# Optimization experiments

Hardware: AMD Instinct MI355X
Metric: run time of the kernel (lower is better)

The kernel has to match this reference:

```python
import jax, jax.numpy as jnp
import numpy as np

EPS = 1e-6
NUM_HEADS = 12


def _layernorm(x, eps=EPS):
    m = jnp.mean(x, axis=-1, keepdims=True)
    v = jnp.var(x, axis=-1, keepdims=True)
    return (x - m) * jax.lax.rsqrt(v + eps)


def _rmsnorm(x, w, eps=EPS):
    ms = jnp.mean(jnp.square(x), axis=-1, keepdims=True)
    return x * jax.lax.rsqrt(ms + eps) * w


def _rope_interleaved(x, cos, sin):
    # x: [B, L, H, hd]; cos/sin: [L, hd//2]; is_neox_style=False (interleaved pairs)
    x1 = x[..., 0::2]
    x2 = x[..., 1::2]
    c = cos[None, :, None, :]
    s = sin[None, :, None, :]
    o1 = x1 * c - x2 * s
    o2 = x1 * s + x2 * c
    return jnp.stack([o1, o2], axis=-1).reshape(x.shape)


def _attention(q, k, v, mask=None):
    # q: [B, Lq, H, hd], k/v: [B, Lk, H, hd]
    hd = q.shape[-1]
    scale = 1.0 / jnp.sqrt(jnp.asarray(hd, q.dtype))
    scores = jnp.einsum('blhd,bmhd->bhlm', q, k) * scale
    if mask is not None:
        scores = jnp.where(mask[None, None], scores, jnp.finfo(scores.dtype).min)
    p = jax.nn.softmax(scores, axis=-1)
    return jnp.einsum('bhlm,bmhd->blhd', p, v)


def setup_inputs() -> dict:
    key = jax.random.key(0)
    B, F, FS, D, FF, LC = 1, 2, 1560, 1536, 8960, 512
    L = F * FS
    hd = D // NUM_HEADS
    ks = jax.random.split(key, 32)
    i = iter(range(32))
    n = lambda shape, s=0.02: jax.random.normal(ks[next(i)], shape, jnp.float32) * s
    inp = {
        'hidden_states': n((B, L, D), 1.0),
        'encoder_hidden_states': n((B, LC, D), 1.0),
        'temb': n((B, F, 6, D), 1.0),
    }
    pos = jnp.arange(L, dtype=jnp.float32)
    inv = 1.0 / (10000.0 ** (jnp.arange(hd // 2, dtype=jnp.float32) / (hd // 2)))
    ang = pos[:, None] * inv[None, :]
    inp['cos'] = jnp.cos(ang)
    inp['sin'] = jnp.sin(ang)
    fidx = jnp.arange(L) // FS
    inp['attn_mask'] = fidx[:, None] >= fidx[None, :]  # frame-level block-causal
    # params
    inp['sst'] = n((1, 6, D), 1.0 / np.sqrt(D))
    for name in ['wq', 'wk', 'wv', 'wo']:
        inp[name] = n((D, D))
    for name in ['bq', 'bk', 'bv', 'bo']:
        inp[name] = jnp.zeros((D,), jnp.float32)
    inp['nq_w'] = jnp.ones((D,), jnp.float32)
    inp['nk_w'] = jnp.ones((D,), jnp.float32)
    inp['ln2_g'] = jnp.ones((D,), jnp.float32)
    inp['ln2_b'] = jnp.zeros((D,), jnp.float32)
    for name in ['cwq', 'cwk', 'cwv', 'cwo']:
        inp[name] = n((D, D))
    for name in ['cbq', 'cbk', 'cbv', 'cbo']:
        inp[name] = jnp.zeros((D,), jnp.float32)
    inp['cnq_w'] = jnp.ones((D,), jnp.float32)
    inp['cnk_w'] = jnp.ones((D,), jnp.float32)
    inp['w1'] = n((D, FF))
    inp['b1'] = jnp.zeros((FF,), jnp.float32)
    inp['w2'] = n((FF, D))
    inp['b2'] = jnp.zeros((D,), jnp.float32)
    return inp


def reference(hidden_states, encoder_hidden_states, temb, cos, sin, attn_mask,
              sst, wq, bq, wk, bk, wv, bv, wo, bo, nq_w, nk_w, ln2_g, ln2_b,
              cwq, cbq, cwk, cbk, cwv, cbv, cwo, cbo, cnq_w, cnk_w,
              w1, b1, w2, b2):
    B, L, D = hidden_states.shape
    F = temb.shape[1]
    FS = L // F
    H = NUM_HEADS
    hd = D // H

    e = sst[:, None] + temb  # [B, F, 6, D]
    shift_msa, scale_msa, gate_msa = e[:, :, 0], e[:, :, 1], e[:, :, 2]
    c_shift, c_scale, c_gate = e[:, :, 3], e[:, :, 4], e[:, :, 5]

    # --- self attention ---
    nh = _layernorm(hidden_states).reshape(B, F, FS, D)
    nh = (nh * (1.0 + scale_msa[:, :, None]) + shift_msa[:, :, None]).reshape(B, L, D)
    q = _rmsnorm(nh @ wq + bq, nq_w).reshape(B, L, H, hd)
    k = _rmsnorm(nh @ wk + bk, nk_w).reshape(B, L, H, hd)
    v = (nh @ wv + bv).reshape(B, L, H, hd)
    q = _rope_interleaved(q, cos, sin)
    k = _rope_interleaved(k, cos, sin)
    attn_out = _attention(q, k, v, attn_mask).reshape(B, L, D) @ wo + bo

    h = hidden_states + (attn_out.reshape(B, F, FS, D) * gate_msa[:, :, None]).reshape(B, L, D)
    norm_h = _layernorm(h) * ln2_g + ln2_b  # null shift/scale

    # --- cross attention ---
    LC = encoder_hidden_states.shape[1]
    cq = _rmsnorm(norm_h @ cwq + cbq, cnq_w).reshape(B, L, H, hd)
    ck = _rmsnorm(encoder_hidden_states @ cwk + cbk, cnk_w).reshape(B, LC, H, hd)
    cv = (encoder_hidden_states @ cwv + cbv).reshape(B, LC, H, hd)
    cross_out = _attention(cq, ck, cv).reshape(B, L, D) @ cwo + cbo

    h = h + cross_out  # gate = 1
    norm_h = _layernorm(h).reshape(B, F, FS, D)
    norm_h = (norm_h * (1.0 + c_scale[:, :, None]) + c_shift[:, :, None]).reshape(B, L, D)

    # --- ffn ---
    ff = jax.nn.gelu(norm_h @ w1 + b1, approximate=True) @ w2 + b2
    h = h + (ff.reshape(B, F, FS, D) * c_gate[:, :, None]).reshape(B, L, D)
    return h
```

## Files before the change

### kernel.cpp

```cpp
#include <hip/hip_runtime.h>
#include <hip/hip_bf16.h>
#include <math.h>

typedef __bf16 bf16;
typedef __bf16 bf16x8 __attribute__((ext_vector_type(8)));
typedef float  f32x4  __attribute__((ext_vector_type(4)));
typedef unsigned int u32;

#define DMODEL 1536
#define NHEADS 12
#define HD 128
#define HDH 64

__device__ __forceinline__ void async16(const void* g, void* l) {
  __builtin_amdgcn_global_load_lds((const __attribute__((address_space(1))) u32*)g,
                                   (__attribute__((address_space(3))) u32*)l, 16, 0, 0);
}

__device__ inline void block_reduce2(float& a, float& b) {
  __shared__ float sa[4], sb[4];
  #pragma unroll
  for (int off = 32; off; off >>= 1) {
    a += __shfl_xor(a, off);
    b += __shfl_xor(b, off);
  }
  int w = threadIdx.x >> 6;
  if ((threadIdx.x & 63) == 0) { sa[w] = a; sb[w] = b; }
  __syncthreads();
  a = sa[0] + sa[1] + sa[2] + sa[3];
  b = sb[0] + sb[1] + sb[2] + sb[3];
  __syncthreads();
}

__global__ __launch_bounds__(256)
void ln_kernel(const float* __restrict__ X, bf16* __restrict__ Y,
               const float* __restrict__ sst, const float* __restrict__ temb,
               const float* __restrict__ g, const float* __restrict__ bvec,
               int jshift, int jscale, int FS, int mode)
{
  int row = blockIdx.x;
  const float* x = X + (size_t)row * DMODEL;
  float v[6];
  float s1 = 0.f, s2 = 0.f;
  #pragma unroll
  for (int i = 0; i < 6; i++) {
    float t = x[threadIdx.x + i * 256];
    v[i] = t; s1 += t; s2 += t * t;
  }
  block_reduce2(s1, s2);
  float mean = s1 * (1.f / DMODEL);
  float var  = s2 * (1.f / DMODEL) - mean * mean;
  float rs = rsqrtf(var + 1e-6f);
  int f = row / FS;
  bf16* y = Y + (size_t)row * DMODEL;
  #pragma unroll
  for (int i = 0; i < 6; i++) {
    int d = threadIdx.x + i * 256;
    float t = (v[i] - mean) * rs;
    float o;
    if (mode == 0) {
      float sc = sst[jscale * DMODEL + d] + temb[(f * 6 + jscale) * DMODEL + d];
      float sh = sst[jshift * DMODEL + d] + temb[(f * 6 + jshift) * DMODEL + d];
      o = t * (1.f + sc) + sh;
    } else {
      o = t * g[d] + bvec[d];
    }
    y[d] = (bf16)o;
  }
}

__global__ __launch_bounds__(256)
void rms_rope_kernel(const float* __restrict__ P, int S, long long MN,
                     const bf16* __restrict__ Xb, int RS, int CO,
                     const float* __restrict__ bias, bf16* __restrict__ Y,
                     const float* __restrict__ w,
                     const float* __restrict__ cosb, const float* __restrict__ sinb,
                     int dorope, float oscale)
{
  __shared__ float rowbuf[DMODEL];
  int row = blockIdx.x;
  float v[6];
  float s2 = 0.f, dummy = 0.f;
  if (Xb) {
    const bf16* x = Xb + (size_t)row * RS + CO;
    #pragma unroll
    for (int i = 0; i < 6; i++) {
      int d = threadIdx.x + i * 256;
      float t = (float)x[d];
      v[i] = t; rowbuf[d] = t; s2 += t * t;
    }
  } else {
    const float* x = P + (size_t)row * RS + CO;
    #pragma unroll
    for (int i = 0; i < 6; i++) {
      int d = threadIdx.x + i * 256;
      float t = bias[d];
      for (int s = 0; s < S; s++) t += x[(size_t)s * MN + d];
      v[i] = t; rowbuf[d] = t; s2 += t * t;
    }
  }
  __syncthreads();
  block_reduce2(s2, dummy);
  float rs = rsqrtf(s2 * (1.f / DMODEL) + 1e-6f) * oscale;
  bf16* y = Y + (size_t)row * DMODEL;
  if (dorope) {
    #pragma unroll
    for (int i = 0; i < 3; i++) {
      int p = threadIdx.x + i * 256;
      int d0 = 2 * p, d1 = 2 * p + 1;
      float y0 = rowbuf[d0] * rs * w[d0];
      float y1 = rowbuf[d1] * rs * w[d1];
      int ih = p & 63;
      float c = cosb[(size_t)row * HDH + ih];
      float s = sinb[(size_t)row * HDH + ih];
      y[d0] = (bf16)(y0 * c - y1 * s);
      y[d1] = (bf16)(y0 * s + y1 * c);
    }
  } else {
    #pragma unroll
    for (int i = 0; i < 6; i++) {
      int d = threadIdx.x + i * 256;
      y[d] = (bf16)(v[i] * rs * w[d]);
    }
  }
}

__global__ __launch_bounds__(256)
void wt_kernel(const float* __restrict__ W, bf16* __restrict__ Wt, int K, int N)
{
  __shared__ float T[32][33];
  int k0 = blockIdx.x * 32, n0 = blockIdx.y * 32;
  int tx = threadIdx.x & 31, ty = threadIdx.x >> 5;
  #pragma unroll
  for (int i = 0; i < 4; i++)
    T[ty + 8 * i][tx] = W[(size_t)(k0 + ty + 8 * i) * N + n0 + tx];
  __syncthreads();
  #pragma unroll
  for (int i = 0; i < 4; i++)
    Wt[(size_t)(n0 + ty + 8 * i) * K + k0 + tx] = (bf16)T[tx][ty + 8 * i];
}

__global__ __launch_bounds__(256)
void catbias_kernel(float* __restrict__ bqkv, const float* __restrict__ bq,
                    const float* __restrict__ bk, const float* __restrict__ bv,
                    float* __restrict__ cbkv, const float* __restrict__ cbk,
                    const float* __restrict__ cbv)
{
  int i = blockIdx.x * 256 + threadIdx.x;
  if (i < DMODEL) {
    bqkv[i] = bq[i]; bqkv[DMODEL + i] = bk[i]; bqkv[2 * DMODEL + i] = bv[i];
    cbkv[i] = cbk[i]; cbkv[DMODEL + i] = cbv[i];
  }
}

__global__ __launch_bounds__(256)
void gemm_bt(const bf16* __restrict__ A, const bf16* __restrict__ Bt,
             const float* __restrict__ bias, float* __restrict__ Cf,
             bf16* __restrict__ Cb, int M, int N, int K, int act,
             int Ks, long long MN)
{
  __shared__ bf16 As[128 * 32];
  __shared__ bf16 Bs[128 * 32];
  int tid = threadIdx.x, lane = tid & 63, w = tid >> 6;
  int wm = w >> 1, wn = w & 1;
  int l16 = lane & 15, quad = lane >> 4;

  int gx = (M + 127) >> 7, gy = N >> 7;
  int per_panel = gx << 3;
  int bid = blockIdx.x;
  int panel = bid / per_panel;
  int rem = bid - panel * per_panel;
  int pc0 = panel << 3;
  int ncols = gy - pc0; if (ncols > 8) ncols = 8;
  int by = pc0 + rem % ncols;
  int bx = rem / ncols;
  int bm = bx * 128, bn = by * 128;

  int kb0 = blockIdx.y * Ks;

  int rl = lane >> 2;
  int kk = (lane & 3) * 8;
  int r0 = (2 * w) * 16 + rl, r1 = (2 * w + 1) * 16 + rl;
  int am0 = bm + r0; if (am0 > M - 1) am0 = M - 1;
  int am1 = bm + r1; if (am1 > M - 1) am1 = M - 1;
  const bf16* a0 = A + (size_t)am0 * K + kk;
  const bf16* a1 = A + (size_t)am1 * K + kk;
  const bf16* b0 = Bt + (size_t)(bn + r0) * K + kk;
  const bf16* b1 = Bt + (size_t)(bn + r1) * K + kk;
  bf16* lA0 = As + (2 * w) * 512; bf16* lA1 = As + (2 * w + 1) * 512;
  bf16* lB0 = Bs + (2 * w) * 512; bf16* lB1 = Bs + (2 * w + 1) * 512;

  f32x4 acc[4][4] = {};
  int kend = kb0 + Ks;
  for (int k0 = kb0; k0 < kend; k0 += 32) {
    async16(a0 + k0, lA0);
    async16(a1 + k0, lA1);
    async16(b0 + k0, lB0);
    async16(b1 + k0, lB1);
    __syncthreads();
    bf16x8 af[4], bfv[4];
    #pragma unroll
    for (int mi = 0; mi < 4; mi++)
      af[mi] = *(const bf16x8*)&As[(wm * 64 + mi * 16 + l16) * 32 + quad * 8];
    #pragma unroll
    for (int ni = 0; ni < 4; ni++)
      bfv[ni] = *(const bf16x8*)&Bs[(wn * 64 + ni * 16 + l16) * 32 + quad * 8];
    #pragma unroll
    for (int mi = 0; mi < 4; mi++)
      #pragma unroll
      for (int ni = 0; ni < 4; ni++)
        acc[mi][ni] = __builtin_amdgcn_mfma_f32_16x16x32_bf16(af[mi], bfv[ni], acc[mi][ni], 0, 0, 0);
    __syncthreads();
  }
  float* Cfo = Cf ? Cf + (size_t)blockIdx.y * MN : nullptr;
  #pragma unroll
  for (int mi = 0; mi < 4; mi++) {
    #pragma unroll
    for (int r = 0; r < 4; r++) {
      int m = bm + wm * 64 + mi * 16 + quad * 4 + r;
      if (m < M) {
        #pragma unroll
        for (int ni = 0; ni < 4; ni++) {
          int n = bn + wn * 64 + ni * 16 + l16;
          float val = acc[mi][ni][r] + (bias ? bias[n] : 0.f);
          if (act == 1) {
            float u = val + 0.044715f * val * val * val;
            float z = 1.5957691216057308f * u;
            val = val / (1.f + __expf(-z));
          }
          if (Cfo) Cfo[(size_t)m * N + n] = val;
          else     Cb[(size_t)m * N + n] = (bf16)val;
        }
      }
    }
  }
}

__global__ __launch_bounds__(256)
void transposev_kernel(const bf16* __restrict__ Xb, int RS, int CO,
                       bf16* __restrict__ Vt, int L)
{
  __shared__ bf16 T[64][65];
  int l0 = blockIdx.x * 64, n0 = blockIdx.y * 64;
  int tid = threadIdx.x;
  int r = tid >> 2;
  int c8 = (tid & 3) * 16;
  int lc = l0 + r; if (lc > L - 1) lc = L - 1;
  const bf16* src = Xb + (size_t)lc * RS + CO + n0 + c8;
  #pragma unroll
  for (int i = 0; i < 16; i++) T[r][c8 + i] = src[i];
  __syncthreads();
  #pragma unroll
  for (int i = 0; i < 16; i++) {
    int l = l0 + c8 + i;
    if (l < L) Vt[(size_t)(n0 + r) * L + l] = T[c8 + i][r];
  }
}

__global__ __launch_bounds__(256)
void flash2_kernel(const bf16* __restrict__ Q, const bf16* __restrict__ Kg,
                   const bf16* __restrict__ Vt, bf16* __restrict__ O,
                   int Lq, int Lk, int FS, int causal, int nqb)
{
  __shared__ bf16 Kt[64 * 128];
  __shared__ bf16 Vtile[128 * 64];
  __shared__ bf16 Pl[4][16][72];
  int tid = threadIdx.x, lane = tid & 63, w = tid >> 6;
  int l16 = lane & 15, quad = lane >> 4;
  int bid = blockIdx.x;
  int h = bid % NHEADS;
  int qb = nqb - 1 - (bid / NHEADS);
  int q0b = qb * 64;
  int q0w = q0b + w * 16;

  int qrow = q0w + l16; if (qrow > Lq - 1) qrow = Lq - 1;
  const bf16* qbase = Q + (size_t)qrow * DMODEL + h * HD + quad * 8;
  bf16x8 qf[4];
  #pragma unroll
  for (int dc = 0; dc < 4; dc++) qf[dc] = *(const bf16x8*)(qbase + dc * 32);

  int kvrow[4];
  int kvmin_w = Lk, kv_end = Lk;
  if (causal) {
    #pragma unroll
    for (int r = 0; r < 4; r++) {
      int qr = q0w + quad * 4 + r; if (qr > Lq - 1) qr = Lq - 1;
      kvrow[r] = (qr / FS + 1) * FS;
    }
    int q0c = q0w; if (q0c > Lq - 1) q0c = Lq - 1;
    kvmin_w = (q0c / FS + 1) * FS;
    int qlast = q0b + 63; if (qlast > Lq - 1) qlast = Lq - 1;
    kv_end = (qlast / FS + 1) * FS;
    if (kv_end > Lk) kv_end = Lk;
  }

  f32x4 acc_o[8] = {};
  float m_i[4], l_i[4];
  #pragma unroll
  for (int r = 0; r < 4; r++) { m_i[r] = -1e30f; l_i[r] = 0.f; }

  for (int kb = 0; kb < kv_end; kb += 64) {
    #pragma unroll
    for (int j = 0; j < 4; j++) {
      int u = w * 256 + j * 64 + lane;
      int row = u >> 4;
      int c = (u & 15) ^ (row & 15);
      int krow = kb + row; if (krow > Lk - 1) krow = Lk - 1;
      async16(Kg + (size_t)krow * DMODEL + h * HD + c * 8,
              Kt + (size_t)(w * 256 + j * 64) * 8);
    }
    #pragma unroll
    for (int j = 0; j < 4; j++) {
      int u = w * 256 + j * 64 + lane;
      int row = u >> 3;
      int c = (u & 7) ^ (row & 7);
      async16(Vt + (size_t)(h * HD + row) * Lk + kb + c * 8,
              Vtile + (size_t)(w * 256 + j * 64) * 8);
    }
    __syncthreads();

    f32x4 s[4] = {};
    #pragma unroll
    for (int nk = 0; nk < 4; nk++) {
      #pragma unroll
      for (int dc = 0; dc < 4; dc++) {
        bf16x8 kf = *(const bf16x8*)&Kt[(((nk * 16 + l16) << 4) + ((4 * dc + quad) ^ l16)) * 8];
        s[nk] = __builtin_amdgcn_mfma_f32_16x16x32_bf16(qf[dc], kf, s[nk], 0, 0, 0);
      }
    }

    bool need_mask = causal && (kb + 64 > kvmin_w);
    float p[4][4];
    #pragma unroll
    for (int r = 0; r < 4; r++) {
      #pragma unroll
      for (int nk = 0; nk < 4; nk++) {
        float sv = s[nk][r];
        if (need_mask && (kb + nk * 16 + l16 >= kvrow[r])) sv = -1e30f;
        p[nk][r] = sv;
      }
      float bm = fmaxf(fmaxf(p[0][r], p[1][r]), fmaxf(p[2][r], p[3][r]));
      #pragma unroll
      for (int off = 8; off; off >>= 1) bm = fmaxf(bm, __shfl_xor(bm, off));
      float mn = fmaxf(m_i[r], bm);
      float alpha = __expf(m_i[r] - mn);
      m_i[r] = mn;
      float ps = 0.f;
      #pragma unroll
      for (int nk = 0; nk < 4; nk++) {
        float e = __expf(p[nk][r] - mn);
        p[nk][r] = e; ps += e;
      }
      #pragma unroll
      for (int off = 8; off; off >>= 1) ps += __shfl_xor(ps, off);
      l_i[r] = l_i[r] * alpha + ps;
      #pragma unroll
      for (int t = 0; t < 8; t++) acc_o[t][r] *= alpha;
    }

    #pragma unroll
    for (int nk = 0; nk < 4; nk++)
      #pragma unroll
      for (int r = 0; r < 4; r++)
        Pl[w][quad * 4 + r][nk * 16 + l16] = (bf16)p[nk][r];
    __threadfence_block();
    bf16x8 pf0 = *(const bf16x8*)&Pl[w][l16][quad * 8];
    bf16x8 pf1 = *(const bf16x8*)&Pl[w][l16][32 + quad * 8];

    #pragma unroll
    for (int t = 0; t < 8; t++) {
      bf16x8 vf0 = *(const bf16x8*)&Vtile[(((t * 16 + l16) << 3) + ((quad) ^ (l16 & 7))) * 8];
      bf16x8 vf1 = *(const bf16x8*)&Vtile[(((t * 16 + l16) << 3) + ((4 + quad) ^ (l16 & 7))) * 8];
      acc_o[t] = __builtin_amdgcn_mfma_f32_16x16x32_bf16(pf0, vf0, acc_o[t], 0, 0, 0);
      acc_o[t] = __builtin_amdgcn_mfma_f32_16x16x32_bf16(pf1, vf1, acc_o[t], 0, 0, 0);
    }
    __syncthreads();
  }

  #pragma unroll
  for (int r = 0; r < 4; r++) {
    int m = q0w + quad * 4 + r;
    if (m < Lq) {
      float inv = 1.f / l_i[r];
      bf16* obase = O + (size_t)m * DMODEL + h * HD;
      #pragma unroll
      for (int t = 0; t < 8; t++)
        obase[t * 16 + l16] = (bf16)(acc_o[t][r] * inv);
    }
  }
}

__global__ __launch_bounds__(256)
void modresid_kernel(const float* __restrict__ base, const float* __restrict__ P,
                     int S, long long MN, const float* __restrict__ bias,
                     float* __restrict__ out,
                     const float* __restrict__ sst, const float* __restrict__ temb,
                     int jg, int FS, long long total)
{
  long long i = (long long)blockIdx.x * 256 + threadIdx.x;
  if (i >= total) return;
  int d = (int)(i % DMODEL);
  int f = (int)((i / DMODEL) / FS);
  float g = sst[jg * DMODEL + d] + temb[(f * 6 + jg) * DMODEL + d];
  float v = bias[d];
  for (int s = 0; s < S; s++) v += P[(size_t)s * MN + i];
  out[i] = base[i] + v * g;
}

__global__ __launch_bounds__(256)
void addf_kernel(float* __restrict__ h, const float* __restrict__ P,
                 int S, long long MN, const float* __restrict__ bias, long long total)
{
  long long i = (long long)blockIdx.x * 256 + threadIdx.x;
  if (i >= total) return;
  int d = (int)(i % DMODEL);
  float v = bias[d];
  for (int s = 0; s < S; s++) v += P[(size_t)s * MN + i];
  h[i] += v;
}

__global__ __launch_bounds__(256)
void cast_kernel(const float* __restrict__ x, bf16* __restrict__ y, long long total)
{
  long long i = (long long)blockIdx.x * 256 + threadIdx.x;
  if (i < total) y[i] = (bf16)x[i];
}

extern "C" void kernel_launch(void* const* d_in, const int* in_sizes, int n_in,
                              void* d_out, int out_size, void* d_ws, size_t ws_size,
                              hipStream_t stream)
{
  const float* hs   = (const float*)d_in[0];
  const float* enc  = (const float*)d_in[1];
  const float* temb = (const float*)d_in[2];
  const float* cosb = (const float*)d_in[3];
  const float* sinb = (const float*)d_in[4];
  const float* sst  = (const float*)d_in[6];
  const float* wq = (const float*)d_in[7];
  const float* wk = (const float*)d_in[8];
  const float* wv = (const float*)d_in[9];
  const float* wo = (const float*)d_in[10];
  const float* bq = (const float*)d_in[11];
  const float* bk = (const float*)d_in[12];
  const float* bv = (const float*)d_in[13];
  const float* bo = (const float*)d_in[14];
  const float* nq_w = (const float*)d_in[15];
  const float* nk_w = (const float*)d_in[16];
  const float* ln2_g = (const float*)d_in[17];
  const float* ln2_b = (const float*)d_in[18];
  const float* cwq = (const float*)d_in[19];
  const float* cwk = (const float*)d_in[20];
  const float* cwv = (const float*)d_in[21];
  const float* cwo = (const float*)d_in[22];
  const float* cbq = (const float*)d_in[23];
  const float* cbk = (const float*)d_in[24];
  const float* cbv = (const float*)d_in[25];
  const float* cbo = (const float*)d_in[26];
  const float* cnq_w = (const float*)d_in[27];
  const float* cnk_w = (const float*)d_in[28];
  const float* w1 = (const float*)d_in[29];
  const float* b1 = (const float*)d_in[30];
  const float* w2 = (const float*)d_in[31];
  const float* b2 = (const float*)d_in[32];

  int L  = in_sizes[0] / DMODEL;
  int LC = in_sizes[1] / DMODEL;
  int F  = in_sizes[2] / (6 * DMODEL);
  int FS = L / F;
  int FF = in_sizes[30];
  long long LD = (long long)L * DMODEL;
  float* outp = (float*)d_out;
  int N3 = 3 * DMODEL, N2 = 2 * DMODEL;

  char* p = (char*)d_ws;
  auto alloc = [&](size_t bytes) -> char* {
    char* r = p; p += (bytes + 255) & ~(size_t)255; return r;
  };
  size_t DD = (size_t)DMODEL * DMODEL;
  bf16* wqkv_t = (bf16*)alloc(DD * 3 * 2);
  bf16* wto_t  = (bf16*)alloc(DD * 2);
  bf16* cwq_t  = (bf16*)alloc(DD * 2);
  bf16* cwkv_t = (bf16*)alloc(DD * 2 * 2);
  bf16* cwo_t  = (bf16*)alloc(DD * 2);
  bf16* w1t = (bf16*)alloc((size_t)DMODEL * FF * 2);
  bf16* w2t = (bf16*)alloc((size_t)DMODEL * FF * 2);
  float* bqkv = (float*)alloc((size_t)N3 * 4);
  float* cbkv = (float*)alloc((size_t)N2 * 4);
  float* hbuf = (float*)alloc((size_t)LD * 4);
  bf16* nh   = (bf16*)alloc((size_t)LD * 2);
  bf16* qb   = (bf16*)alloc((size_t)LD * 2);
  bf16* kb   = (bf16*)alloc((size_t)LD * 2);
  bf16* ab   = (bf16*)alloc((size_t)LD * 2);
  bf16* vtc  = (bf16*)alloc((size_t)LC * DMODEL * 2);
  bf16* encb = (bf16*)alloc((size_t)LC * DMODEL * 2);
  char* BIG1 = alloc((size_t)L * FF * 2);
  bf16* qkvb = (bf16*)BIG1;
  bf16* ckvb = (bf16*)BIG1;
  bf16* ffb  = (bf16*)BIG1;
  char* BIG2 = alloc((size_t)LD * 2 * 4);
  bf16* vtb = (bf16*)BIG2;
  float* Pp = (float*)BIG2;
  (void)ws_size; (void)n_in; (void)out_size;

  dim3 gWdd(DMODEL / 32, DMODEL / 32);
  wt_kernel<<<gWdd, 256, 0, stream>>>(wq, wqkv_t, DMODEL, DMODEL);
  wt_kernel<<<gWdd, 256, 0, stream>>>(wk, wqkv_t + DD, DMODEL, DMODEL);
  wt_kernel<<<gWdd, 256, 0, stream>>>(wv, wqkv_t + 2 * DD, DMODEL, DMODEL);
  wt_kernel<<<gWdd, 256, 0, stream>>>(wo, wto_t, DMODEL, DMODEL);
  wt_kernel<<<gWdd, 256, 0, stream>>>(cwq, cwq_t, DMODEL, DMODEL);
  wt_kernel<<<gWdd, 256, 0, stream>>>(cwk, cwkv_t, DMODEL, DMODEL);
  wt_kernel<<<gWdd, 256, 0, stream>>>(cwv, cwkv_t + DD, DMODEL, DMODEL);
  wt_kernel<<<gWdd, 256, 0, stream>>>(cwo, cwo_t, DMODEL, DMODEL);
  wt_kernel<<<dim3(DMODEL / 32, FF / 32), 256, 0, stream>>>(w1, w1t, DMODEL, FF);
  wt_kernel<<<dim3(FF / 32, DMODEL / 32), 256, 0, stream>>>(w2, w2t, FF, DMODEL);
  catbias_kernel<<<6, 256, 0, stream>>>(bqkv, bq, bk, bv, cbkv, cbk, cbv);

  int gxL = (L + 127) / 128, gxC = (LC + 127) / 128;
  int ewg = (int)((LD + 255) / 256);
  int nqb = (L + 63) / 64;
  const float qs = 0.08838834764831845f;

  ln_kernel<<<L, 256, 0, stream>>>(hs, nh, sst, temb, nullptr, nullptr, 0, 1, FS, 0);
  gemm_bt<<<dim3(gxL * (N3 / 128), 1), 256, 0, stream>>>(nh, wqkv_t, bqkv, nullptr, qkvb,
                                                         L, N3, DMODEL, 0, DMODEL, 0);
  rms_rope_kernel<<<L, 256, 0, stream>>>(nullptr, 0, 0, qkvb, N3, 0, nullptr, qb, nq_w, cosb, sinb, 1, qs);
  rms_rope_kernel<<<L, 256, 0, stream>>>(nullptr, 0, 0, qkvb, N3, DMODEL, nullptr, kb, nk_w, cosb, sinb, 1, 1.0f);
  transposev_kernel<<<dim3((L + 63) / 64, DMODEL / 64), 256, 0, stream>>>(qkvb, N3, 2 * DMODEL, vtb, L);
  flash2_kernel<<<NHEADS * nqb, 256, 0, stream>>>(qb, kb, vtb, ab, L, L, FS, 1, nqb);
  gemm_bt<<<dim3(gxL * (DMODEL / 128), 2), 256, 0, stream>>>(ab, wto_t, nullptr, Pp, nullptr,
                                                             L, DMODEL, DMODEL, 0, DMODEL / 2, LD);
  modresid_kernel<<<ewg, 256, 0, stream>>>(hs, Pp, 2, LD, bo, hbuf, sst, temb, 2, FS, LD);
  ln_kernel<<<L, 256, 0, stream>>>(hbuf, nh, nullptr, nullptr, ln2_g, ln2_b, 0, 0, FS, 1);
  gemm_bt<<<dim3(gxL * (DMODEL / 128), 2), 256, 0, stream>>>(nh, cwq_t, nullptr, Pp, nullptr,
                                                             L, DMODEL, DMODEL, 0, DMODEL / 2, LD);
  rms_rope_kernel<<<L, 256, 0, stream>>>(Pp, 2, LD, nullptr, DMODEL, 0, cbq, qb, cnq_w, nullptr, nullptr, 0, qs);
  cast_kernel<<<(int)(((long long)LC * DMODEL + 255) / 256), 256, 0, stream>>>(enc, encb, (long long)LC * DMODEL);
  gemm_bt<<<dim3(gxC * (N2 / 128), 1), 256, 0, stream>>>(encb, cwkv_t, cbkv, nullptr, ckvb,
                                                         LC, N2, DMODEL, 0, DMODEL, 0);
  rms_rope_kernel<<<LC, 256, 0, stream>>>(nullptr, 0, 0, ckvb, N2, 0, nullptr, kb, cnk_w, nullptr, nullptr, 0, 1.0f);
  transposev_kernel<<<dim3((LC + 63) / 64, DMODEL / 64), 256, 0, stream>>>(ckvb, N2, DMODEL, vtc, LC);
  flash2_kernel<<<NHEADS * nqb, 256, 0, stream>>>(qb, kb, vtc, ab, L, LC, FS, 0, nqb);
  gemm_bt<<<dim3(gxL * (DMODEL / 128), 2), 256, 0, stream>>>(ab, cwo_t, nullptr, Pp, nullptr,
                                                             L, DMODEL, DMODEL, 0, DMODEL / 2, LD);
  addf_kernel<<<ewg, 256, 0, stream>>>(hbuf, Pp, 2, LD, cbo, LD);
  ln_kernel<<<L, 256, 0, stream>>>(hbuf, nh, sst, temb, nullptr, nullptr, 3, 4, FS, 0);
  gemm_bt<<<dim3(gxL * (FF / 128), 1), 256, 0, stream>>>(nh, w1t, b1, nullptr, ffb,
                                                         L, FF, DMODEL, 1, DMODEL, 0);
  gemm_bt<<<dim3(gxL * (DMODEL / 128), 2), 256, 0, stream>>>(ffb, w2t, nullptr, Pp, nullptr,
                                                             L, DMODEL, FF, 0, FF / 2, LD);
  modresid_kernel<<<ewg, 256, 0, stream>>>(hbuf, Pp, 2, LD, b2, outp, sst, temb, 5, FS, LD);
}
```

Baseline: 1.226 ms.

## Add 256x256-tile pipelined MFMA GEMM and route all large GEMMs through it

Introduces a 512-thread GEMM kernel with 256x256 output tiles and 64-wide K steps. It double-buffers A/B tiles in LDS using async global-to-LDS loads with an XOR swizzle, and interleaves the loads with MFMA phases under s_setprio and explicit waitcnt/barriers. All QKV, projection and FFN GEMMs now use it instead of the 128x128 kernel. The larger tiles give more data reuse per block but produce far fewer blocks, some wasted rows since 3120 does not divide by 256, and about 128KB of LDS per block, so occupancy and CU fill may suffer on the D=1536 GEMMs.

```diff
diff --git a/kernel.cpp b/kernel.cpp
--- a/kernel.cpp
+++ b/kernel.cpp
@@ -218,6 +218,162 @@
     #pragma unroll
     for (int r = 0; r < 4; r++) {
       int m = bm + wm * 64 + mi * 16 + quad * 4 + r;
+      if (m < M) {
+        #pragma unroll
+        for (int ni = 0; ni < 4; ni++) {
+          int n = bn + wn * 64 + ni * 16 + l16;
+          float val = acc[mi][ni][r] + (bias ? bias[n] : 0.f);
+          if (act == 1) {
+            float u = val + 0.044715f * val * val * val;
+            float z = 1.5957691216057308f * u;
+            val = val / (1.f + __expf(-z));
+          }
+          if (Cfo) Cfo[(size_t)m * N + n] = val;
+          else     Cb[(size_t)m * N + n] = (bf16)val;
+        }
+      }
+    }
+  }
+}
+
+__global__ __launch_bounds__(512, 2)
+void gemm256(const bf16* __restrict__ A, const bf16* __restrict__ Bt,
+             const float* __restrict__ bias, float* __restrict__ Cf,
+             bf16* __restrict__ Cb, int M, int N, int K, int act,
+             int Ks, long long MN)
+{
+  __shared__ bf16 LDS[2][2][128 * 128];
+  int tid = threadIdx.x, lane = tid & 63, w = tid >> 6;
+  int wm = w >> 2, wn = w & 3;
+  int l16 = lane & 15, quad = lane >> 4;
+
+  int gmx = (M + 255) >> 8;
+  int bx = blockIdx.x % gmx, by = blockIdx.x / gmx;
+  int bm = bx << 8, bn = by << 8;
+  int kb0 = blockIdx.y * Ks;
+  int NT = Ks >> 6;
+
+  int aro = (l16 * 64 + quad * 16) ^ ((l16 >> 3) << 5);
+  const char* A0r = (const char*)&LDS[0][0][0] + wm * 16384 + aro;
+  const char* A1r = (const char*)&LDS[1][0][0] + wm * 16384 + aro;
+  const char* B0r = (const char*)&LDS[0][1][0] + wn * 8192 + aro;
+  const char* B1r = (const char*)&LDS[1][1][0] + wn * 8192 + aro;
+
+  int srl = lane >> 2;
+  int sc16 = (lane & 3) ^ (((lane >> 5) & 1) << 1);
+  int Mm1 = M - 1, Nm1 = N - 1;
+  int ga0 = bm + w * 16 + srl;        if (ga0 > Mm1) ga0 = Mm1;
+  int ga1 = bm + 128 + w * 16 + srl;  if (ga1 > Mm1) ga1 = Mm1;
+  int gb0 = bn + w * 16 + srl;        if (gb0 > Nm1) gb0 = Nm1;
+  int gb1 = bn + 128 + w * 16 + srl;  if (gb1 > Nm1) gb1 = Nm1;
+  const bf16* Ag0 = A + (size_t)ga0 * K + sc16 * 8;
+  const bf16* Ag1 = A + (size_t)ga1 * K + sc16 * 8;
+  const bf16* Bg0 = Bt + (size_t)gb0 * K + sc16 * 8;
+  const bf16* Bg1 = Bt + (size_t)gb1 * K + sc16 * 8;
+  char* wA0[2] = { (char*)&LDS[0][0][0] + w * 2048, (char*)&LDS[1][0][0] + w * 2048 };
+  char* wA1[2] = { wA0[0] + 16384, wA0[1] + 16384 };
+  char* wB0[2] = { (char*)&LDS[0][1][0] + w * 2048, (char*)&LDS[1][1][0] + w * 2048 };
+  char* wB1[2] = { wB0[0] + 16384, wB0[1] + 16384 };
+
+#define STG(src, kk_, dst) do { const bf16* _s = (src) + (kk_); \
+    async16(_s, (dst)); async16(_s + 32, (dst) + 1024); } while (0)
+#define MFMA_(d, a, b) d = __builtin_amdgcn_mfma_f32_16x16x32_bf16(a, b, d, 0, 0, 0)
+
+  STG(Ag0, kb0, wA0[0]); STG(Ag1, kb0, wA1[0]);
+  STG(Bg0, kb0, wB0[0]); STG(Bg1, kb0, wB1[0]);
+  if (NT > 1) {
+    STG(Bg0, kb0 + 64, wB0[1]); STG(Bg1, kb0 + 64, wB1[1]);
+    asm volatile("s_waitcnt vmcnt(4)" ::: "memory");
+  } else {
+    asm volatile("s_waitcnt vmcnt(0)" ::: "memory");
+  }
+  __builtin_amdgcn_s_barrier();
+
+  f32x4 acc[8][4] = {};
+  for (int t = 0; t < NT; ++t) {
+    int b = t & 1;
+    const char* Ab = b ? A1r : A0r;
+    const char* Bb = b ? B1r : B0r;
+    int kt1 = kb0 + (t + 1) * 64;
+    int kt2 = kt1 + 64;
+    bool st1 = (t + 1) < NT, st2 = (t + 2) < NT;
+
+    bf16x8 a0[8], b0v[4];
+    #pragma unroll
+    for (int i = 0; i < 8; i++) a0[i] = *(const bf16x8*)(Ab + i * 1024);
+    #pragma unroll
+    for (int i = 0; i < 4; i++) b0v[i] = *(const bf16x8*)(Bb + i * 1024);
+    if (st1) STG(Ag0, kt1, wA0[b ^ 1]);
+    __builtin_amdgcn_s_barrier();
+    asm volatile("s_waitcnt lgkmcnt(0)" ::: "memory");
+    __builtin_amdgcn_s_setprio(1);
+    #pragma unroll
+    for (int mi = 0; mi < 4; mi++)
+      #pragma unroll
+      for (int ni = 0; ni < 2; ni++) {
+        MFMA_(acc[mi][ni], a0[mi * 2],     b0v[ni * 2]);
+        MFMA_(acc[mi][ni], a0[mi * 2 + 1], b0v[ni * 2 + 1]);
+      }
+    __builtin_amdgcn_s_setprio(0);
+    __builtin_amdgcn_s_barrier();
+
+    bf16x8 b1v[4];
+    #pragma unroll
+    for (int i = 0; i < 4; i++) b1v[i] = *(const bf16x8*)(Bb + (4 + i) * 1024);
+    if (st1) STG(Ag1, kt1, wA1[b ^ 1]);
+    __builtin_amdgcn_s_barrier();
+    asm volatile("s_waitcnt lgkmcnt(0)" ::: "memory");
+    __builtin_amdgcn_s_setprio(1);
+    #pragma unroll
+    for (int mi = 0; mi < 4; mi++)
+      #pragma unroll
+      for (int ni = 0; ni < 2; ni++) {
+        MFMA_(acc[mi][2 + ni], a0[mi * 2],     b1v[ni * 2]);
+        MFMA_(acc[mi][2 + ni], a0[mi * 2 + 1], b1v[ni * 2 + 1]);
+      }
+    __builtin_amdgcn_s_setprio(0);
+    __builtin_amdgcn_s_barrier();
+
+    bf16x8 a1[8];
+    #pragma unroll
+    for (int i = 0; i < 8; i++) a1[i] = *(const bf16x8*)(Ab + (8 + i) * 1024);
+    if (st2) STG(Bg0, kt2, wB0[b]);
+    __builtin_amdgcn_s_barrier();
+    asm volatile("s_waitcnt lgkmcnt(0)" ::: "memory");
+    __builtin_amdgcn_s_setprio(1);
+    #pragma unroll
+    for (int mi = 0; mi < 4; mi++)
+      #pragma unroll
+      for (int ni = 0; ni < 2; ni++) {
+        MFMA_(acc[4 + mi][2 + ni], a1[mi * 2],     b1v[ni * 2]);
+        MFMA_(acc[4 + mi][2 + ni], a1[mi * 2 + 1], b1v[ni * 2 + 1]);
+      }
+    __builtin_amdgcn_s_setprio(0);
+    __builtin_amdgcn_s_barrier();
+
+    if (st2) STG(Bg1, kt2, wB1[b]);
+    __builtin_amdgcn_s_setprio(1);
+    #pragma unroll
+    for (int mi = 0; mi < 4; mi++)
+      #pragma unroll
+      for (int ni = 0; ni < 2; ni++) {
+        MFMA_(acc[4 + mi][ni], a1[mi * 2],     b0v[ni * 2]);
+        MFMA_(acc[4 + mi][ni], a1[mi * 2 + 1], b0v[ni * 2 + 1]);
+      }
+    __builtin_amdgcn_s_setprio(0);
+    if (st2)      { asm volatile("s_waitcnt vmcnt(4)" ::: "memory"); }
+    else if (st1) { asm volatile("s_waitcnt vmcnt(0)" ::: "memory"); }
+    __builtin_amdgcn_s_barrier();
+  }
+#undef STG
+#undef MFMA_
+
+  float* Cfo = Cf ? Cf + (size_t)blockIdx.y * MN : nullptr;
+  #pragma unroll
+  for (int mi = 0; mi < 8; mi++) {
+    #pragma unroll
+    for (int r = 0; r < 4; r++) {
+      int m = bm + wm * 128 + mi * 16 + quad * 4 + r;
       if (m < M) {
         #pragma unroll
         for (int ni = 0; ni < 4; ni++) {
@@ -515,23 +671,24 @@
   wt_kernel<<<dim3(FF / 32, DMODEL / 32), 256, 0, stream>>>(w2, w2t, FF, DMODEL);
   catbias_kernel<<<6, 256, 0, stream>>>(bqkv, bq, bk, bv, cbkv, cbk, cbv);
 
-  int gxL = (L + 127) / 128, gxC = (LC + 127) / 128;
+  int gxC = (LC + 127) / 128;
+  int gmx = (L + 255) / 256;
   int ewg = (int)((LD + 255) / 256);
   int nqb = (L + 63) / 64;
   const float qs = 0.08838834764831845f;
 
   ln_kernel<<<L, 256, 0, stream>>>(hs, nh, sst, temb, nullptr, nullptr, 0, 1, FS, 0);
-  gemm_bt<<<dim3(gxL * (N3 / 128), 1), 256, 0, stream>>>(nh, wqkv_t, bqkv, nullptr, qkvb,
+  gemm256<<<dim3(gmx * (N3 / 256), 1), 512, 0, stream>>>(nh, wqkv_t, bqkv, nullptr, qkvb,
                                                          L, N3, DMODEL, 0, DMODEL, 0);
   rms_rope_kernel<<<L, 256, 0, stream>>>(nullptr, 0, 0, qkvb, N3, 0, nullptr, qb, nq_w, cosb, sinb, 1, qs);
   rms_rope_kernel<<<L, 256, 0, stream>>>(nullptr, 0, 0, qkvb, N3, DMODEL, nullptr, kb, nk_w, cosb, sinb, 1, 1.0f);
   transposev_kernel<<<dim3((L + 63) / 64, DMODEL / 64), 256, 0, stream>>>(qkvb, N3, 2 * DMODEL, vtb, L);
   flash2_kernel<<<NHEADS * nqb, 256, 0, stream>>>(qb, kb, vtb, ab, L, L, FS, 1, nqb);
-  gemm_bt<<<dim3(gxL * (DMODEL / 128), 2), 256, 0, stream>>>(ab, wto_t, nullptr, Pp, nullptr,
+  gemm256<<<dim3(gmx * (DMODEL / 256), 2), 512, 0, stream>>>(ab, wto_t, nullptr, Pp, nullptr,
                                                              L, DMODEL, DMODEL, 0, DMODEL / 2, LD);
   modresid_kernel<<<ewg, 256, 0, stream>>>(hs, Pp, 2, LD, bo, hbuf, sst, temb, 2, FS, LD);
   ln_kernel<<<L, 256, 0, stream>>>(hbuf, nh, nullptr, nullptr, ln2_g, ln2_b, 0, 0, FS, 1);
-  gemm_bt<<<dim3(gxL * (DMODEL / 128), 2), 256, 0, stream>>>(nh, cwq_t, nullptr, Pp, nullptr,
+  gemm256<<<dim3(gmx * (DMODEL / 256), 2), 512, 0, stream>>>(nh, cwq_t, nullptr, Pp, nullptr,
                                                              L, DMODEL, DMODEL, 0, DMODEL / 2, LD);
   rms_rope_kernel<<<L, 256, 0, stream>>>(Pp, 2, LD, nullptr, DMODEL, 0, cbq, qb, cnq_w, nullptr, nullptr, 0, qs);
   cast_kernel<<<(int)(((long long)LC * DMODEL + 255) / 256), 256, 0, stream>>>(enc, encb, (long long)LC * DMODEL);
@@ -540,13 +697,13 @@
   rms_rope_kernel<<<LC, 256, 0, stream>>>(nullptr, 0, 0, ckvb, N2, 0, nullptr, kb, cnk_w, nullptr, nullptr, 0, 1.0f);
   transposev_kernel<<<dim3((LC + 63) / 64, DMODEL / 64), 256, 0, stream>>>(ckvb, N2, DMODEL, vtc, LC);
   flash2_kernel<<<NHEADS * nqb, 256, 0, stream>>>(qb, kb, vtc, ab, L, LC, FS, 0, nqb);
-  gemm_bt<<<dim3(gxL * (DMODEL / 128), 2), 256, 0, stream>>>(ab, cwo_t, nullptr, Pp, nullptr,
+  gemm256<<<dim3(gmx * (DMODEL / 256), 2), 512, 0, stream>>>(ab, cwo_t, nullptr, Pp, nullptr,
                                                              L, DMODEL, DMODEL, 0, DMODEL / 2, LD);
   addf_kernel<<<ewg, 256, 0, stream>>>(hbuf, Pp, 2, LD, cbo, LD);
   ln_kernel<<<L, 256, 0, stream>>>(hbuf, nh, sst, temb, nullptr, nullptr, 3, 4, FS, 0);
-  gemm_bt<<<dim3(gxL * (FF / 128), 1), 256, 0, stream>>>(nh, w1t, b1, nullptr, ffb,
+  gemm256<<<dim3(gmx * (FF / 256), 1), 512, 0, stream>>>(nh, w1t, b1, nullptr, ffb,
                                                          L, FF, DMODEL, 1, DMODEL, 0);
-  gemm_bt<<<dim3(gxL * (DMODEL / 128), 2), 256, 0, stream>>>(ffb, w2t, nullptr, Pp, nullptr,
+  gemm256<<<dim3(gmx * (DMODEL / 256), 2), 512, 0, stream>>>(ffb, w2t, nullptr, Pp, nullptr,
                                                              L, DMODEL, FF, 0, FF / 2, LD);
   modresid_kernel<<<ewg, 256, 0, stream>>>(hbuf, Pp, 2, LD, b2, outp, sst, temb, 5, FS, LD);
 }
```

Result: faster. 1.157 ms (-5.6%).

## Triple-buffer GEMM LDS loads with swizzled layout and three-way split-K

Applied to the files above, without the earlier changes.

Replaces the single-buffered GEMM, which synchronized twice per K step, with a 3-stage LDS ring. Async global-to-LDS loads run two tiles ahead, gated by explicit vmcnt waits and one barrier per iteration. The LDS layout is XOR-swizzled to reduce bank conflicts, and occupancy is hinted at 3 blocks per CU. Split-K for the N=1536 GEMMs goes from 2 to 3 partial slices to raise CU utilization, at the cost of a larger fp32 partial buffer and extra reduction traffic in the downstream elementwise kernels.

```diff
diff --git a/kernel.cpp b/kernel.cpp
--- a/kernel.cpp
+++ b/kernel.cpp
@@ -153,14 +153,13 @@
   }
 }
 
-__global__ __launch_bounds__(256)
-void gemm_bt(const bf16* __restrict__ A, const bf16* __restrict__ Bt,
+__global__ __launch_bounds__(256, 3)
+void gemm128(const bf16* __restrict__ A, const bf16* __restrict__ Bt,
              const float* __restrict__ bias, float* __restrict__ Cf,
              bf16* __restrict__ Cb, int M, int N, int K, int act,
-             int Ks, long long MN)
-{
-  __shared__ bf16 As[128 * 32];
-  __shared__ bf16 Bs[128 * 32];
+             int S, long long MN)
+{
+  __shared__ bf16 LDS[3][2][4096];
   int tid = threadIdx.x, lane = tid & 63, w = tid >> 6;
   int wm = w >> 1, wn = w & 1;
   int l16 = lane & 15, quad = lane >> 4;
@@ -174,44 +173,66 @@
   int ncols = gy - pc0; if (ncols > 8) ncols = 8;
   int by = pc0 + rem % ncols;
   int bx = rem / ncols;
-  int bm = bx * 128, bn = by * 128;
-
-  int kb0 = blockIdx.y * Ks;
-
-  int rl = lane >> 2;
-  int kk = (lane & 3) * 8;
-  int r0 = (2 * w) * 16 + rl, r1 = (2 * w + 1) * 16 + rl;
-  int am0 = bm + r0; if (am0 > M - 1) am0 = M - 1;
-  int am1 = bm + r1; if (am1 > M - 1) am1 = M - 1;
-  const bf16* a0 = A + (size_t)am0 * K + kk;
-  const bf16* a1 = A + (size_t)am1 * K + kk;
-  const bf16* b0 = Bt + (size_t)(bn + r0) * K + kk;
-  const bf16* b1 = Bt + (size_t)(bn + r1) * K + kk;
-  bf16* lA0 = As + (2 * w) * 512; bf16* lA1 = As + (2 * w + 1) * 512;
-  bf16* lB0 = Bs + (2 * w) * 512; bf16* lB1 = Bs + (2 * w + 1) * 512;
+  int bm = bx << 7, bn = by << 7;
+
+  int NTtot = K >> 5;
+  int sidx = blockIdx.y;
+  int basek = NTtot / S, remk = NTtot % S;
+  int NT = basek + (sidx < remk ? 1 : 0);
+  int t0k = sidx * basek + (sidx < remk ? sidx : remk);
+  int kb0 = t0k << 5;
+
+  int aro = (l16 * 64 + quad * 16) ^ ((l16 >> 3) << 5);
+  char* ldsb = (char*)&LDS[0][0][0];
+
+  int srl = lane >> 2;
+  int sc16 = (lane & 3) ^ (((lane >> 5) & 1) << 1);
+  int Mm1 = M - 1, Nm1 = N - 1;
+  int ga0 = bm + w * 16 + srl;       if (ga0 > Mm1) ga0 = Mm1;
+  int ga1 = bm + 64 + w * 16 + srl;  if (ga1 > Mm1) ga1 = Mm1;
+  int gb0 = bn + w * 16 + srl;       if (gb0 > Nm1) gb0 = Nm1;
+  int gb1 = bn + 64 + w * 16 + srl;  if (gb1 > Nm1) gb1 = Nm1;
+  const bf16* Ag0 = A + (size_t)ga0 * K + kb0 + sc16 * 8;
+  const bf16* Ag1 = A + (size_t)ga1 * K + kb0 + sc16 * 8;
+  const bf16* Bg0 = Bt + (size_t)gb0 * K + kb0 + sc16 * 8;
+  const bf16* Bg1 = Bt + (size_t)gb1 * K + kb0 + sc16 * 8;
+
+#define STG(tt) do { int _k = (tt) * 32; \
+    char* _d = ldsb + ((tt) % 3) * 16384 + w * 1024; \
+    async16(Ag0 + _k, _d);         async16(Ag1 + _k, _d + 4096); \
+    async16(Bg0 + _k, _d + 8192);  async16(Bg1 + _k, _d + 12288); } while (0)
+#define MFMA_(d, a, b) d = __builtin_amdgcn_mfma_f32_16x16x32_bf16(a, b, d, 0, 0, 0)
+
+  STG(0);
+  if (NT > 1) STG(1);
+  if (NT > 1) { asm volatile("s_waitcnt vmcnt(4)" ::: "memory"); }
+  else        { asm volatile("s_waitcnt vmcnt(0)" ::: "memory"); }
+  __builtin_amdgcn_s_barrier();
 
   f32x4 acc[4][4] = {};
-  int kend = kb0 + Ks;
-  for (int k0 = kb0; k0 < kend; k0 += 32) {
-    async16(a0 + k0, lA0);
-    async16(a1 + k0, lA1);
-    async16(b0 + k0, lB0);
-    async16(b1 + k0, lB1);
-    __syncthreads();
+  for (int t = 0; t < NT; ++t) {
+    if (t + 2 < NT) STG(t + 2);
+    const char* Ar = ldsb + (t % 3) * 16384 + wm * 4096 + aro;
+    const char* Br = ldsb + (t % 3) * 16384 + 8192 + wn * 4096 + aro;
     bf16x8 af[4], bfv[4];
     #pragma unroll
+    for (int i = 0; i < 4; i++) bfv[i] = *(const bf16x8*)(Br + i * 1024);
+    #pragma unroll
+    for (int i = 0; i < 4; i++) af[i] = *(const bf16x8*)(Ar + i * 1024);
+    #pragma unroll
     for (int mi = 0; mi < 4; mi++)
-      af[mi] = *(const bf16x8*)&As[(wm * 64 + mi * 16 + l16) * 32 + quad * 8];
-    #pragma unroll
-    for (int ni = 0; ni < 4; ni++)
-      bfv[ni] = *(const bf16x8*)&Bs[(wn * 64 + ni * 16 + l16) * 32 + quad * 8];
-    #pragma unroll
-    for (int mi = 0; mi < 4; mi++)
       #pragma unroll
       for (int ni = 0; ni < 4; ni++)
-        acc[mi][ni] = __builtin_amdgcn_mfma_f32_16x16x32_bf16(af[mi], bfv[ni], acc[mi][ni], 0, 0, 0);
-    __syncthreads();
-  }
+        MFMA_(acc[mi][ni], af[mi], bfv[ni]);
+    if (t + 1 < NT) {
+      if (t + 2 < NT) { asm volatile("s_waitcnt vmcnt(4)" ::: "memory"); }
+      else            { asm volatile("s_waitcnt vmcnt(0)" ::: "memory"); }
+      __builtin_amdgcn_s_barrier();
+    }
+  }
+#undef STG
+#undef MFMA_
+
   float* Cfo = Cf ? Cf + (size_t)blockIdx.y * MN : nullptr;
   #pragma unroll
   for (int mi = 0; mi < 4; mi++) {
@@ -497,7 +518,7 @@
   bf16* qkvb = (bf16*)BIG1;
   bf16* ckvb = (bf16*)BIG1;
   bf16* ffb  = (bf16*)BIG1;
-  char* BIG2 = alloc((size_t)LD * 2 * 4);
+  char* BIG2 = alloc((size_t)LD * 3 * 4);
   bf16* vtb = (bf16*)BIG2;
   float* Pp = (float*)BIG2;
   (void)ws_size; (void)n_in; (void)out_size;
@@ -515,38 +536,39 @@
   wt_kernel<<<dim3(FF / 32, DMODEL / 32), 256, 0, stream>>>(w2, w2t, FF, DMODEL);
   catbias_kernel<<<6, 256, 0, stream>>>(bqkv, bq, bk, bv, cbkv, cbk, cbv);
 
-  int gxL = (L + 127) / 128, gxC = (LC + 127) / 128;
+  int gxL = (L + 127) / 128;
+  int gxC = (LC + 127) / 128;
   int ewg = (int)((LD + 255) / 256);
   int nqb = (L + 63) / 64;
   const float qs = 0.08838834764831845f;
 
   ln_kernel<<<L, 256, 0, stream>>>(hs, nh, sst, temb, nullptr, nullptr, 0, 1, FS, 0);
-  gemm_bt<<<dim3(gxL * (N3 / 128), 1), 256, 0, stream>>>(nh, wqkv_t, bqkv, nullptr, qkvb,
-                                                         L, N3, DMODEL, 0, DMODEL, 0);
+  gemm128<<<dim3(gxL * (N3 / 128), 1), 256, 0, stream>>>(nh, wqkv_t, bqkv, nullptr, qkvb,
+                                                         L, N3, DMODEL, 0, 1, 0);
   rms_rope_kernel<<<L, 256, 0, stream>>>(nullptr, 0, 0, qkvb, N3, 0, nullptr, qb, nq_w, cosb, sinb, 1, qs);
   rms_rope_kernel<<<L, 256, 0, stream>>>(nullptr, 0, 0, qkvb, N3, DMODEL, nullptr, kb, nk_w, cosb, sinb, 1, 1.0f);
   transposev_kernel<<<dim3((L + 63) / 64, DMODEL / 64), 256, 0, stream>>>(qkvb, N3, 2 * DMODEL, vtb, L);
   flash2_kernel<<<NHEADS * nqb, 256, 0, stream>>>(qb, kb, vtb, ab, L, L, FS, 1, nqb);
-  gemm_bt<<<dim3(gxL * (DMODEL / 128), 2), 256, 0, stream>>>(ab, wto_t, nullptr, Pp, nullptr,
-                                                             L, DMODEL, DMODEL, 0, DMODEL / 2, LD);
-  modresid_kernel<<<ewg, 256, 0, stream>>>(hs, Pp, 2, LD, bo, hbuf, sst, temb, 2, FS, LD);
+  gemm128<<<dim3(gxL * (DMODEL / 128), 3), 256, 0, stream>>>(ab, wto_t, nullptr, Pp, nullptr,
+                                                             L, DMODEL, DMODEL, 0, 3, LD);
+  modresid_kernel<<<ewg, 256, 0, stream>>>(hs, Pp, 3, LD, bo, hbuf, sst, temb, 2, FS, LD);
   ln_kernel<<<L, 256, 0, stream>>>(hbuf, nh, nullptr, nullptr, ln2_g, ln2_b, 0, 0, FS, 1);
-  gemm_bt<<<dim3(gxL * (DMODEL / 128), 2), 256, 0, stream>>>(nh, cwq_t, nullptr, Pp, nullptr,
-                                                             L, DMODEL, DMODEL, 0, DMODEL / 2, LD);
-  rms_rope_kernel<<<L, 256, 0, stream>>>(Pp, 2, LD, nullptr, DMODEL, 0, cbq, qb, cnq_w, nullptr, nullptr, 0, qs);
+  gemm128<<<dim3(gxL * (DMODEL / 128), 3), 256, 0, stream>>>(nh, cwq_t, nullptr, Pp, nullptr,
+                                                             L, DMODEL, DMODEL, 0, 3, LD);
+  rms_rope_kernel<<<L, 256, 0, stream>>>(Pp, 3, LD, nullptr, DMODEL, 0, cbq, qb, cnq_w, nullptr, nullptr, 0, qs);
   cast_kernel<<<(int)(((long long)LC * DMODEL + 255) / 256), 256, 0, stream>>>(enc, encb, (long long)LC * DMODEL);
-  gemm_bt<<<dim3(gxC * (N2 / 128), 1), 256, 0, stream>>>(encb, cwkv_t, cbkv, nullptr, ckvb,
-                                                         LC, N2, DMODEL, 0, DMODEL, 0);
+  gemm128<<<dim3(gxC * (N2 / 128), 1), 256, 0, stream>>>(encb, cwkv_t, cbkv, nullptr, ckvb,
+                                                         LC, N2, DMODEL, 0, 1, 0);
   rms_rope_kernel<<<LC, 256, 0, stream>>>(nullptr, 0, 0, ckvb, N2, 0, nullptr, kb, cnk_w, nullptr, nullptr, 0, 1.0f);
   transposev_kernel<<<dim3((LC + 63) / 64, DMODEL / 64), 256, 0, stream>>>(ckvb, N2, DMODEL, vtc, LC);
   flash2_kernel<<<NHEADS * nqb, 256, 0, stream>>>(qb, kb, vtc, ab, L, LC, FS, 0, nqb);
-  gemm_bt<<<dim3(gxL * (DMODEL / 128), 2), 256, 0, stream>>>(ab, cwo_t, nullptr, Pp, nullptr,
-                                                             L, DMODEL, DMODEL, 0, DMODEL / 2, LD);
-  addf_kernel<<<ewg, 256, 0, stream>>>(hbuf, Pp, 2, LD, cbo, LD);
+  gemm128<<<dim3(gxL * (DMODEL / 128), 3), 256, 0, stream>>>(ab, cwo_t, nullptr, Pp, nullptr,
+                                                             L, DMODEL, DMODEL, 0, 3, LD);
+  addf_kernel<<<ewg, 256, 0, stream>>>(hbuf, Pp, 3, LD, cbo, LD);
   ln_kernel<<<L, 256, 0, stream>>>(hbuf, nh, sst, temb, nullptr, nullptr, 3, 4, FS, 0);
-  gemm_bt<<<dim3(gxL * (FF / 128), 1), 256, 0, stream>>>(nh, w1t, b1, nullptr, ffb,
-                                                         L, FF, DMODEL, 1, DMODEL, 0);
-  gemm_bt<<<dim3(gxL * (DMODEL / 128), 2), 256, 0, stream>>>(ffb, w2t, nullptr, Pp, nullptr,
-                                                             L, DMODEL, FF, 0, FF / 2, LD);
-  modresid_kernel<<<ewg, 256, 0, stream>>>(hbuf, Pp, 2, LD, b2, outp, sst, temb, 5, FS, LD);
-}
+  gemm128<<<dim3(gxL * (FF / 128), 1), 256, 0, stream>>>(nh, w1t, b1, nullptr, ffb,
+                                                         L, FF, DMODEL, 1, 1, 0);
+  gemm128<<<dim3(gxL * (DMODEL / 128), 3), 256, 0, stream>>>(ffb, w2t, nullptr, Pp, nullptr,
+                                                             L, DMODEL, FF, 0, 3, LD);
+  modresid_kernel<<<ewg, 256, 0, stream>>>(hbuf, Pp, 3, LD, b2, outp, sst, temb, 5, FS, LD);
+}
```

Measured after the change: 1.167 ms. -4.8%, faster.
